# Kernel optimization log

Hardware: AMD Instinct MI355X
Metric: run time of the kernel (lower is better)

Reference implementation:

```python
import jax, jax.numpy as jnp
import numpy as np

B, S, E, H, Dh, R, L = 32, 512, 512, 8, 64, 3, 2
NI, NS = 10000, 1000
SCALE = float(1.0 / np.sqrt(Dh))
NEG = -1000000000.0


def _tensor_attn(q, kv, Wq, bq, Wk, bk, Wv, bv, Wg, bg, Wtq, btq, Wtk, btk, core, mask):
    # q, kv: [B,S,E]
    Q = q @ Wq + bq
    K = kv @ Wk + bk
    V = kv @ Wv + bv
    # per-query global bias computed from full key projection: [B,S,H] -> [B,H,S,1]
    glo = jnp.transpose(K @ Wg + bg, (0, 2, 1))[..., None]
    Qh = Q.reshape(B, S, H, Dh).transpose(0, 2, 1, 3)  # [B,H,S,Dh]
    Kh = K.reshape(B, S, H, Dh).transpose(0, 2, 1, 3)
    Vh = V.reshape(B, S, H, Dh).transpose(0, 2, 1, 3)
    scores = jnp.einsum('bhqd,bhkd->bhqk', Qh, Kh)  # [B,H,S,S]
    # low-rank bilinear tensor-core term; note it depends only on position s
    qt = Qh @ Wtq + btq  # [B,H,S,R]
    kt = Kh @ Wtk + btk  # [B,H,S,R]
    ts = jnp.einsum('bhsi,ij,bhsj->bhs', qt, core, kt)  # [B,H,S]
    scores = (scores + glo + ts[..., None]) * SCALE
    scores = jnp.where(mask, NEG, scores)
    p = jax.nn.softmax(scores, axis=-1)
    out = jnp.einsum('bhqk,bhkd->bhqd', p, Vh)
    return out.transpose(0, 2, 1, 3).reshape(B, S, E)


def setup_inputs() -> dict:
    key = jax.random.key(0)
    ks = jax.random.split(key, 24)
    f = lambda k, shp, s=0.02: (jax.random.normal(k, shp, dtype=jnp.float32) * s)
    inp = {}
    inp['item_inputs'] = jax.random.randint(ks[0], (B, S), 0, NI)
    inp['skill_inputs'] = jax.random.randint(ks[1], (B, S), 0, NS)
    inp['label_inputs'] = jax.random.randint(ks[2], (B, S), 0, 2)
    inp['item_ids'] = jax.random.randint(ks[3], (B, S), 0, NI)
    inp['skill_ids'] = jax.random.randint(ks[4], (B, S), 0, NS)
    inp['item_emb'] = f(ks[5], (NI + 1, E // 2), 1.0).at[0].set(0.0)  # padding_idx=0
    inp['skill_emb'] = f(ks[6], (NS + 1, E // 2), 1.0).at[0].set(0.0)
    inp['W_in'] = f(ks[7], (2 * E, E))
    inp['b_in'] = jnp.zeros((E,), jnp.float32)
    inp['Wq'] = f(ks[8], (L, E, E))
    inp['bq'] = jnp.zeros((L, E), jnp.float32)
    inp['Wk'] = f(ks[9], (L, E, E))
    inp['bk'] = jnp.zeros((L, E), jnp.float32)
    inp['Wv'] = f(ks[10], (L, E, E))
    inp['bv'] = jnp.zeros((L, E), jnp.float32)
    inp['Wg'] = f(ks[11], (L, E, H))
    inp['bg'] = jnp.zeros((L, H), jnp.float32)
    inp['Wtq'] = f(ks[12], (L, Dh, R), 0.1)
    inp['btq'] = jnp.zeros((L, R), jnp.float32)
    inp['Wtk'] = f(ks[13], (L, Dh, R), 0.1)
    inp['btk'] = jnp.zeros((L, R), jnp.float32)
    inp['core'] = f(ks[14], (L, R, R), 0.5)
    inp['W_out'] = f(ks[15], (E, 1))
    inp['b_out'] = jnp.zeros((1,), jnp.float32)
    return inp


def reference(item_inputs, skill_inputs, label_inputs, item_ids, skill_ids,
              item_emb, skill_emb, W_in, b_in, Wq, bq, Wk, bk, Wv, bv,
              Wg, bg, Wtq, btq, Wtk, btk, core, W_out, b_out):
    # get_inputs
    ie = item_emb[item_inputs]    # [B,S,E/2]
    se = skill_emb[skill_inputs]
    lab = label_inputs[..., None].astype(jnp.float32)
    half = jnp.concatenate([ie, se], axis=-1)  # [B,S,E]
    inputs = jnp.concatenate([half * lab, half * (1.0 - lab)], axis=-1)  # [B,S,2E]
    x = jax.nn.relu(inputs @ W_in + b_in)  # [B,S,E]
    # query
    query = jnp.concatenate([item_emb[item_ids], skill_emb[skill_ids]], axis=-1)
    mask = jnp.triu(jnp.ones((1, 1, S, S), dtype=bool), k=1)
    out = _tensor_attn(query, x, Wq[0], bq[0], Wk[0], bk[0], Wv[0], bv[0],
                       Wg[0], bg[0], Wtq[0], btq[0], Wtk[0], btk[0], core[0], mask)
    for l in range(1, L):
        res = _tensor_attn(query, out, Wq[l], bq[l], Wk[l], bk[l], Wv[l], bv[l],
                           Wg[l], bg[l], Wtq[l], btq[l], Wtk[l], btk[l], core[l], mask)
        out = out + jax.nn.relu(res)
    return out @ W_out + b_out  # [B,S,1]
```

## Files before the change

kernel.cpp:

```cpp
#include <hip/hip_runtime.h>
#include <stdint.h>


typedef short short8v __attribute__((ext_vector_type(8)));
typedef float f32x4 __attribute__((ext_vector_type(4)));

__device__ __forceinline__ float bf2f(unsigned short u) {
  union { unsigned int i; float f; } c;
  c.i = ((unsigned int)u) << 16;
  return c.f;
}
__device__ __forceinline__ unsigned short f2bf(float f) {
  union { float f; unsigned int i; } c;
  c.f = f;
  unsigned int u = c.i + 0x7FFFu + ((c.i >> 16) & 1u);
  return (unsigned short)(u >> 16);
}

__device__ __forceinline__ void g2l16(const void* g, void* l) {
  __builtin_amdgcn_global_load_lds(
      (const __attribute__((address_space(1))) unsigned int*)g,
      (__attribute__((address_space(3))) unsigned int*)l, 16, 0, 0);
}

struct WPtrs {
  const float* s[7];
  unsigned short* d[7];
};
__global__ __launch_bounds__(256) void transpose_all_k(WPtrs p, int* __restrict__ iperm) {
  int by = blockIdx.y;
  if (by == 0) {
    int gid = blockIdx.x * 256 + threadIdx.x;
    for (int i = gid; i < 16512; i += 4096) iperm[i] = 16384 + (i & 127);
  }
  __shared__ float t[32][33];
  int mi, r0t;
  if (by < 32) { mi = 0; r0t = by; }
  else { mi = 1 + ((by - 32) >> 4); r0t = (by - 32) & 15; }
  const float* in = p.s[mi];
  unsigned short* out = p.d[mi];
  int R = (mi == 0) ? 1024 : 512;
  const int C = 512;
  int c0 = blockIdx.x * 32, r0 = r0t * 32;
  int lr = threadIdx.x >> 5, lc = threadIdx.x & 31;
#pragma unroll
  for (int i = 0; i < 4; ++i) {
    int r = lr + i * 8;
    t[r][lc] = in[(size_t)(r0 + r) * C + (c0 + lc)];
  }
  __syncthreads();
#pragma unroll
  for (int i = 0; i < 4; ++i) {
    int r = lr + i * 8;
    out[(size_t)(c0 + r) * R + (r0 + lc)] = f2bf(t[lc][r]);
  }
}

__global__ __launch_bounds__(256) void scan_k(const int* __restrict__ label_in,
                                              int* __restrict__ iperm,
                                              int* __restrict__ rowpos,
                                              int* __restrict__ cnt) {
  __shared__ int sc[256];
  int t = threadIdx.x;
  int c = 0;
#pragma unroll 16
  for (int i = 0; i < 64; ++i) c += label_in[t * 64 + i];
  sc[t] = c;
  __syncthreads();
  for (int off = 1; off < 256; off <<= 1) {
    int v = sc[t];
    int u = (t >= off) ? sc[t - off] : 0;
    __syncthreads();
    sc[t] = v + u;
    __syncthreads();
  }
  int inc = sc[t];
  int ex = inc - c;
  int ex0 = t * 64 - ex;
  int p1 = ex;
  int p0 = 16511 - ex0;
  for (int i = 0; i < 64; ++i) {
    int row = t * 64 + i;
    int lb = label_in[row];
    int pos = lb ? (p1++) : (p0--);
    iperm[pos] = row;
    rowpos[row] = pos;
  }
  if (t == 255) cnt[0] = sc[255];
}

__global__ __launch_bounds__(256) void build_inputs_k(
    const int* __restrict__ item_in, const int* __restrict__ skill_in,
    const int* __restrict__ item_id, const int* __restrict__ skill_id,
    const float* __restrict__ iemb, const float* __restrict__ semb,
    unsigned short* __restrict__ HALFC, unsigned short* __restrict__ QRY,
    const int* __restrict__ rowpos) {
  int w = threadIdx.x >> 6, lane = threadIdx.x & 63;
  int row = blockIdx.x * 4 + w;
  int ii = item_in[row], si = skill_in[row];
  int iq = item_id[row], sq = skill_id[row];
  int pos = rowpos[row];
  int c = lane * 8;
  const float* src = (c < 256) ? (iemb + (size_t)ii * 256 + c)
                               : (semb + (size_t)si * 256 + (c - 256));
  union { unsigned short u[8]; int4 v; } o;
#pragma unroll
  for (int i = 0; i < 8; ++i) o.u[i] = f2bf(src[i]);
  *(int4*)(HALFC + (size_t)pos * 512 + c) = o.v;
  int qc = lane * 8;
  const float* qs = (qc < 256) ? (iemb + (size_t)iq * 256 + qc)
                               : (semb + (size_t)sq * 256 + (qc - 256));
  union { unsigned short u[8]; int4 v; } q;
#pragma unroll
  for (int i = 0; i < 8; ++i) q.u[i] = f2bf(qs[i]);
  *(int4*)(QRY + (size_t)row * 512 + qc) = q.v;
}

#define CT_LD 132

__global__ __launch_bounds__(256, 4) void gemm_q_in_k(
    const unsigned short* __restrict__ QRY, const unsigned short* __restrict__ WqTC,
    unsigned short* __restrict__ Qb, const unsigned short* __restrict__ HALFC,
    const unsigned short* __restrict__ WInT, unsigned short* __restrict__ X,
    const int* __restrict__ iperm, const int* __restrict__ cnt,
    const float* __restrict__ b_in, const float* __restrict__ bq, float SC) {
  __shared__ __align__(16) unsigned short uS[128 * CT_LD];
  int bid = blockIdx.x;
  int tid = threadIdx.x;
  int w = tid >> 6, lane = tid & 63, l16 = lane & 15, quad = lane >> 4;
  if (bid < 1024) {
    unsigned short* sA = uS;
    unsigned short* sB = uS + 128 * 64;
    unsigned short* Ct = uS;
    int mb = bid & 127, nb = bid >> 7;
    int wm = w & 1, wn = w >> 1;
    f32x4 acc[4][4];
#pragma unroll
    for (int i = 0; i < 4; ++i)
#pragma unroll
      for (int j = 0; j < 4; ++j) acc[i][j] = (f32x4){0.f, 0.f, 0.f, 0.f};
    for (int k0 = 0; k0 < 512; k0 += 64) {
      __syncthreads();
#pragma unroll
      for (int jj = 0; jj < 4; ++jj) {
        int c = jj * 256 + tid;
        int row = c >> 3, kc = c & 7, src = kc ^ (row & 7);
        g2l16(QRY + (size_t)(mb * 128 + row) * 512 + k0 + src * 8, sA + (size_t)c * 8);
      }
#pragma unroll
      for (int jj = 0; jj < 4; ++jj) {
        int c = jj * 256 + tid;
        int row = c >> 3, kc = c & 7, src = kc ^ (row & 7);
        g2l16(WqTC + (size_t)(nb * 128 + row) * 512 + k0 + src * 8, sB + (size_t)c * 8);
      }
      __syncthreads();
#pragma unroll
      for (int kk = 0; kk < 2; ++kk) {
        short8v aF[4], bF[4];
#pragma unroll
        for (int mt = 0; mt < 4; ++mt) {
          int r = wm * 64 + mt * 16 + l16;
          aF[mt] = *(const short8v*)(sA + r * 64 + (((kk * 4 + quad) ^ (r & 7)) << 3));
        }
#pragma unroll
        for (int nt = 0; nt < 4; ++nt) {
          int r = wn * 64 + nt * 16 + l16;
          bF[nt] = *(const short8v*)(sB + r * 64 + (((kk * 4 + quad) ^ (r & 7)) << 3));
        }
#pragma unroll
        for (int mt = 0; mt < 4; ++mt)
#pragma unroll
          for (int nt = 0; nt < 4; ++nt)
            acc[mt][nt] =
                __builtin_amdgcn_mfma_f32_16x16x32_bf16(aF[mt], bF[nt], acc[mt][nt], 0, 0, 0);
      }
    }
    __syncthreads();
#pragma unroll
    for (int mt = 0; mt < 4; ++mt)
#pragma unroll
      for (int nt = 0; nt < 4; ++nt) {
        int col = wn * 64 + nt * 16 + l16;
        float bs = bq[nb * 128 + col];
#pragma unroll
        for (int r = 0; r < 4; ++r) {
          int row = wm * 64 + mt * 16 + quad * 4 + r;
          Ct[row * CT_LD + col] = f2bf((acc[mt][nt][r] + bs) * SC);
        }
      }
    __syncthreads();
#pragma unroll
    for (int it = 0; it < 8; ++it) {
      int row = it * 16 + (tid >> 4);
      int col8 = (tid & 15) * 8;
      *(int4*)(Qb + (size_t)(mb * 128 + row) * 1024 + nb * 128 + col8) =
          *(const int4*)(Ct + row * CT_LD + col8);
    }
  } else {
    unsigned short* sA = uS;
    unsigned short* sB = uS + 64 * 64;
    unsigned short* Ct = uS;
    int id = bid - 1024;
    int nb = id / 264, mb = id % 264;
    if (mb >= 258) return;
    int n1 = *cnt;
    int koff = (mb < ((n1 + 63) >> 6)) ? 0 : 512;
    f32x4 acc[4][2];
#pragma unroll
    for (int i = 0; i < 4; ++i)
#pragma unroll
      for (int j = 0; j < 2; ++j) acc[i][j] = (f32x4){0.f, 0.f, 0.f, 0.f};
    for (int k0 = 0; k0 < 512; k0 += 64) {
      __syncthreads();
#pragma unroll
      for (int jj = 0; jj < 2; ++jj) {
        int c = jj * 256 + tid;
        int row = c >> 3, kc = c & 7, src = kc ^ (row & 7);
        g2l16(HALFC + (size_t)(mb * 64 + row) * 512 + k0 + src * 8, sA + (size_t)c * 8);
      }
#pragma unroll
      for (int jj = 0; jj < 4; ++jj) {
        int c = jj * 256 + tid;
        int row = c >> 3, kc = c & 7, src = kc ^ (row & 7);
        g2l16(WInT + (size_t)(nb * 128 + row) * 1024 + koff + k0 + src * 8, sB + (size_t)c * 8);
      }
      __syncthreads();
#pragma unroll
      for (int kk = 0; kk < 2; ++kk) {
        short8v aF[4], bF[2];
#pragma unroll
        for (int mt = 0; mt < 4; ++mt) {
          int r = mt * 16 + l16;
          aF[mt] = *(const short8v*)(sA + r * 64 + (((kk * 4 + quad) ^ (r & 7)) << 3));
        }
#pragma unroll
        for (int nt = 0; nt < 2; ++nt) {
          int r = w * 32 + nt * 16 + l16;
          bF[nt] = *(const short8v*)(sB + r * 64 + (((kk * 4 + quad) ^ (r & 7)) << 3));
        }
#pragma unroll
        for (int mt = 0; mt < 4; ++mt)
#pragma unroll
          for (int nt = 0; nt < 2; ++nt)
            acc[mt][nt] =
                __builtin_amdgcn_mfma_f32_16x16x32_bf16(aF[mt], bF[nt], acc[mt][nt], 0, 0, 0);
      }
    }
    __syncthreads();
#pragma unroll
    for (int mt = 0; mt < 4; ++mt)
#pragma unroll
      for (int nt = 0; nt < 2; ++nt) {
        int col = w * 32 + nt * 16 + l16;
        float bs = b_in[nb * 128 + col];
#pragma unroll
        for (int r = 0; r < 4; ++r) {
          int row = mt * 16 + quad * 4 + r;
          Ct[row * CT_LD + col] = f2bf(fmaxf(acc[mt][nt][r] + bs, 0.f));
        }
      }
    __syncthreads();
#pragma unroll
    for (int it = 0; it < 4; ++it) {
      int row = it * 16 + (tid >> 4);
      int tgt = iperm[mb * 64 + row];
      int col8 = (tid & 15) * 8;
      *(int4*)(X + (size_t)tgt * 512 + nb * 128 + col8) = *(const int4*)(Ct + row * CT_LD + col8);
    }
  }
}

__global__ __launch_bounds__(256, 4) void gemm_bt_k(
    const unsigned short* __restrict__ A, const unsigned short* __restrict__ Bt,
    unsigned short* __restrict__ C, int K, int ldc,
    const float* __restrict__ biasA, const float* __restrict__ biasB,
    int nsplit, float scale, unsigned short* __restrict__ VTout,
    float* __restrict__ dstfill, const float* __restrict__ bout) {
  __shared__ __align__(16) unsigned short uS[128 * CT_LD];
  unsigned short* sA = uS;
  unsigned short* sB = uS + 128 * 64;
  unsigned short* Ct = uS;
  int mb = blockIdx.x, nb = blockIdx.y;
  int tid = threadIdx.x;
  int w = tid >> 6, lane = tid & 63, l16 = lane & 15, quad = lane >> 4;
  int wm = w & 1, wn = w >> 1;
  if (dstfill && nb == 0 && tid < 128) dstfill[mb * 128 + tid] = bout[0];
  f32x4 acc[4][4];
#pragma unroll
  for (int i = 0; i < 4; ++i)
#pragma unroll
    for (int jn = 0; jn < 4; ++jn) acc[i][jn] = (f32x4){0.f, 0.f, 0.f, 0.f};

  for (int k0 = 0; k0 < K; k0 += 64) {
    __syncthreads();
#pragma unroll
    for (int jj = 0; jj < 4; ++jj) {
      int c = jj * 256 + tid;
      int row = c >> 3, kc = c & 7, src = kc ^ (row & 7);
      g2l16(A + (size_t)(mb * 128 + row) * K + k0 + src * 8, sA + (size_t)c * 8);
    }
#pragma unroll
    for (int jj = 0; jj < 4; ++jj) {
      int c = jj * 256 + tid;
      int row = c >> 3, kc = c & 7, src = kc ^ (row & 7);
      g2l16(Bt + (size_t)(nb * 128 + row) * K + k0 + src * 8, sB + (size_t)c * 8);
    }
    __syncthreads();
#pragma unroll
    for (int kk = 0; kk < 2; ++kk) {
      short8v aF[4], bF[4];
#pragma unroll
      for (int mt = 0; mt < 4; ++mt) {
        int r = wm * 64 + mt * 16 + l16;
        aF[mt] = *(const short8v*)(sA + r * 64 + (((kk * 4 + quad) ^ (r & 7)) << 3));
      }
#pragma unroll
      for (int nt = 0; nt < 4; ++nt) {
        int r = wn * 64 + nt * 16 + l16;
        bF[nt] = *(const short8v*)(sB + r * 64 + (((kk * 4 + quad) ^ (r & 7)) << 3));
      }
#pragma unroll
      for (int mt = 0; mt < 4; ++mt)
#pragma unroll
        for (int nt = 0; nt < 4; ++nt)
          acc[mt][nt] =
              __builtin_amdgcn_mfma_f32_16x16x32_bf16(aF[mt], bF[nt], acc[mt][nt], 0, 0, 0);
    }
  }
  __syncthreads();
#pragma unroll
  for (int mt = 0; mt < 4; ++mt)
#pragma unroll
    for (int nt = 0; nt < 4; ++nt) {
      int col = wn * 64 + nt * 16 + l16;
      int gcol = nb * 128 + col;
      float bs = (gcol < nsplit) ? biasA[gcol] : biasB[gcol - nsplit];
#pragma unroll
      for (int r = 0; r < 4; ++r) {
        int row = wm * 64 + mt * 16 + quad * 4 + r;
        Ct[row * CT_LD + col] = f2bf((acc[mt][nt][r] + bs) * scale);
      }
    }
  __syncthreads();
  if (VTout && nb >= 4) {
    int bb = mb >> 2, kpb = (mb & 3) * 128;
#pragma unroll
    for (int it = 0; it < 8; ++it) {
      int idx = it * 256 + tid;
      int dloc = idx >> 4, rem = idx & 15;
      union { unsigned short u[8]; int4 v; } o;
#pragma unroll
      for (int s = 0; s < 8; ++s) {
        int r = 32 * (rem >> 2) + 16 * (s >> 2) + 4 * (rem & 3) + (s & 3);
        o.u[s] = Ct[r * CT_LD + dloc];
      }
      *(int4*)(VTout + (size_t)(bb * 512 + (nb - 4) * 128 + dloc) * 512 + kpb + rem * 8) = o.v;
    }
  } else {
#pragma unroll
    for (int it = 0; it < 8; ++it) {
      int row = it * 16 + (tid >> 4);
      int col8 = (tid & 15) * 8;
      *(int4*)(C + (size_t)(mb * 128 + row) * ldc + nb * 128 + col8) =
          *(const int4*)(Ct + row * CT_LD + col8);
    }
  }
}

template <int FINAL>
__global__ __launch_bounds__(256, 4) void attn_k(const unsigned short* __restrict__ Qb,
                                                 int ldq,
                                                 const unsigned short* __restrict__ KVb,
                                                 const unsigned short* __restrict__ VT,
                                                 unsigned short* __restrict__ Out,
                                                 const unsigned short* __restrict__ out0,
                                                 const float* __restrict__ wout,
                                                 float* __restrict__ dst) {
  __shared__ __align__(16) unsigned short sK[64 * 64];
  __shared__ __align__(16) unsigned short sV[64 * 64];
  int tid = threadIdx.x;
  int w = tid >> 6, lane = tid & 63;
  int l16 = lane & 15, quad = lane >> 4;
  int bh = blockIdx.x;
  int b = bh >> 3, h = bh & 7;
  int jb = 7 - (int)blockIdx.y;
  int qb = jb * 64 + w * 16;
  f32x4 zf = {0.f, 0.f, 0.f, 0.f};
  short8v onesF;
#pragma unroll
  for (int i = 0; i < 8; ++i) onesF[i] = (short)0x3F80;

  short8v qF[2];
#pragma unroll
  for (int hf = 0; hf < 2; ++hf)
    qF[hf] = *(const short8v*)(Qb + (size_t)(b * 512 + qb + l16) * ldq + h * 64 + hf * 32 +
                               quad * 8);

  f32x4 O[4], RS = zf;
#pragma unroll
  for (int dt = 0; dt < 4; ++dt) O[dt] = zf;

  const unsigned short* Kg = KVb + (size_t)(b * 512) * 1024 + h * 64;
  const unsigned short* Vg = VT + (size_t)(bh * 64) * 512;

  for (int kt = 0; kt <= jb; ++kt) {
    __syncthreads();
#pragma unroll
    for (int jj = 0; jj < 2; ++jj) {
      int c = jj * 256 + tid;
      int row = c >> 3, kc = c & 7, src = kc ^ (row & 7);
      g2l16(Kg + (size_t)(kt * 64 + row) * 1024 + src * 8, sK + c * 8);
    }
#pragma unroll
    for (int jj = 0; jj < 2; ++jj) {
      int c = jj * 256 + tid;
      int row = c >> 3, kc = c & 7, src = kc ^ (row & 7);
      g2l16(Vg + (size_t)row * 512 + kt * 64 + src * 8, sV + c * 8);
    }
    __syncthreads();
#pragma unroll
    for (int kp = 0; kp < 2; ++kp) {
      int kb32 = kt * 64 + kp * 32;
      if (kb32 > qb) continue;
      short8v kC[2][2], vC[4];
#pragma unroll
      for (int v = 0; v < 2; ++v) {
        int r = kp * 32 + v * 16 + l16;
#pragma unroll
        for (int hf = 0; hf < 2; ++hf)
          kC[v][hf] = *(const short8v*)(sK + r * 64 + (((hf * 4 + quad) ^ (r & 7)) << 3));
      }
#pragma unroll
      for (int dt = 0; dt < 4; ++dt) {
        int r = dt * 16 + l16;
        vC[dt] = *(const short8v*)(sV + r * 64 + (((kp * 4 + quad) ^ (r & 7)) << 3));
      }
      f32x4 S[2];
#pragma unroll
      for (int v = 0; v < 2; ++v) {
        f32x4 s0 = __builtin_amdgcn_mfma_f32_16x16x32_bf16(kC[v][0], qF[0], zf, 0, 0, 0);
        S[v] = __builtin_amdgcn_mfma_f32_16x16x32_bf16(kC[v][1], qF[1], s0, 0, 0, 0);
      }
      if (kb32 + 31 > qb) {
#pragma unroll
        for (int v = 0; v < 2; ++v)
#pragma unroll
          for (int r = 0; r < 4; ++r)
            if (kb32 + v * 16 + quad * 4 + r > qb + l16) S[v][r] = -1e30f;
      }
      union { unsigned int u32[4]; short8v v8; } pk;
#pragma unroll
      for (int i = 0; i < 4; ++i) {
        int v = i >> 1, r0 = (i & 1) * 2;
        float e0 = __expf(S[v][r0]);
        float e1 = __expf(S[v][r0 + 1]);
        pk.u32[i] = (__float_as_uint(e0) >> 16) | (__float_as_uint(e1) & 0xFFFF0000u);
      }
#pragma unroll
      for (int dt = 0; dt < 4; ++dt)
        O[dt] = __builtin_amdgcn_mfma_f32_16x16x32_bf16(pk.v8, vC[dt], O[dt], 0, 0, 0);
      RS = __builtin_amdgcn_mfma_f32_16x16x32_bf16(pk.v8, onesF, RS, 0, 0, 0);
    }
  }
  float lr[4];
#pragma unroll
  for (int r = 0; r < 4; ++r) lr[r] = 1.f / RS[r];
  if (!FINAL) {
#pragma unroll
    for (int dt = 0; dt < 4; ++dt)
#pragma unroll
      for (int r = 0; r < 4; ++r)
        Out[(size_t)(b * 512 + qb + quad * 4 + r) * 512 + h * 64 + dt * 16 + l16] =
            f2bf(O[dt][r] * lr[r]);
  } else {
    float s[4] = {0.f, 0.f, 0.f, 0.f};
#pragma unroll
    for (int dt = 0; dt < 4; ++dt) {
      float wv = wout[h * 64 + dt * 16 + l16];
#pragma unroll
      for (int r = 0; r < 4; ++r) {
        float rv = bf2f(f2bf(O[dt][r] * lr[r]));
        float oo = bf2f(out0[(size_t)(b * 512 + qb + quad * 4 + r) * 512 + h * 64 +
                             dt * 16 + l16]);
        s[r] += (oo + fmaxf(rv, 0.f)) * wv;
      }
    }
#pragma unroll
    for (int off = 1; off < 16; off <<= 1)
#pragma unroll
      for (int r = 0; r < 4; ++r) s[r] += __shfl_xor(s[r], off);
    if (l16 == 0) {
#pragma unroll
      for (int r = 0; r < 4; ++r)
        atomicAdd(dst + b * 512 + qb + quad * 4 + r, s[r]);
    }
  }
}

extern "C" void kernel_launch(void* const* d_in, const int* in_sizes, int n_in,
                              void* d_out, int out_size, void* d_ws, size_t ws_size,
                              hipStream_t stream) {
  (void)in_sizes; (void)n_in; (void)out_size; (void)ws_size;
  const int* item_inputs = (const int*)d_in[0];
  const int* skill_inputs = (const int*)d_in[1];
  const int* label_inputs = (const int*)d_in[2];
  const int* item_ids = (const int*)d_in[3];
  const int* skill_ids = (const int*)d_in[4];
  const float* item_emb = (const float*)d_in[5];
  const float* skill_emb = (const float*)d_in[6];
  const float* W_in = (const float*)d_in[7];
  const float* b_in = (const float*)d_in[8];
  const float* Wq = (const float*)d_in[9];
  const float* bq = (const float*)d_in[10];
  const float* Wk = (const float*)d_in[11];
  const float* bk = (const float*)d_in[12];
  const float* Wv = (const float*)d_in[13];
  const float* bv = (const float*)d_in[14];
  const float* W_out = (const float*)d_in[22];
  const float* b_out = (const float*)d_in[23];

  unsigned short* ws = (unsigned short*)d_ws;
  unsigned short* HALFC = ws;
  unsigned short* OUT0 = ws;
  unsigned short* QRY = ws + (size_t)16512 * 512;
  unsigned short* X = QRY + (size_t)16384 * 512;
  unsigned short* Qb = X + (size_t)16512 * 512;
  unsigned short* KVb = Qb + (size_t)16384 * 1024;
  unsigned short* WInT = KVb + (size_t)16384 * 1024;
  unsigned short* WqTC = WInT + 512 * 1024;
  unsigned short* WkvT0 = WqTC + (size_t)1024 * 512;
  unsigned short* WkvT1 = WkvT0 + (size_t)1024 * 512;
  unsigned short* VT = WkvT1 + (size_t)1024 * 512;
  int* IPERM = (int*)(VT + (size_t)16384 * 512);
  int* CNT = IPERM + 16512;
  int* ROWPOS = CNT + 2;

  WPtrs p;
  p.s[0] = W_in;           p.d[0] = WInT;
  p.s[1] = Wq;             p.d[1] = WqTC;
  p.s[2] = Wq + 262144;    p.d[2] = WqTC + 512 * 512;
  p.s[3] = Wk;             p.d[3] = WkvT0;
  p.s[4] = Wv;             p.d[4] = WkvT0 + 262144;
  p.s[5] = Wk + 262144;    p.d[5] = WkvT1;
  p.s[6] = Wv + 262144;    p.d[6] = WkvT1 + 262144;
  transpose_all_k<<<dim3(16, 128), 256, 0, stream>>>(p, IPERM);

  scan_k<<<1, 256, 0, stream>>>(label_inputs, IPERM, ROWPOS, CNT);

  build_inputs_k<<<4096, 256, 0, stream>>>(item_inputs, skill_inputs, item_ids, skill_ids,
                                           item_emb, skill_emb, HALFC, QRY, ROWPOS);

  const float SC = 0.125f;
  gemm_q_in_k<<<2080, 256, 0, stream>>>(QRY, WqTC, Qb, HALFC, WInT, X, IPERM, CNT, b_in, bq,
                                        SC);
  gemm_bt_k<<<dim3(128, 8), 256, 0, stream>>>(X, WkvT0, KVb, 512, 1024, bk, bv, 512, 1.0f,
                                              VT, nullptr, nullptr);
  attn_k<0><<<dim3(256, 8), 256, 0, stream>>>(Qb, 1024, KVb, VT, OUT0, nullptr, nullptr,
                                              nullptr);
  gemm_bt_k<<<dim3(128, 8), 256, 0, stream>>>(OUT0, WkvT1, KVb, 512, 1024, bk + 512,
                                              bv + 512, 512, 1.0f, VT, (float*)d_out, b_out);
  attn_k<1><<<dim3(256, 8), 256, 0, stream>>>(Qb + 512, 1024, KVb, VT, nullptr, OUT0, W_out,
                                              (float*)d_out);
}
```

Baseline: 257.2 us.

## Double-buffer attention K/V tiles and merge transpose with input-build launch

The attention kernel now uses two LDS buffers for K and V. It issues the global-to-LDS loads for the next tile before computing the current one, using explicit vmcnt waits, barriers and setprio so load latency overlaps with MFMA work. The weight transpose and embedding gather kernels are merged into one launch. The iperm padding init moves into the scan kernel so it only fills the tail entries. This removes one kernel launch and a per-tile load stall, at the cost of doubling attention LDS use, which may reduce occupancy.

```diff
diff --git a/kernel.cpp b/kernel.cpp
--- a/kernel.cpp
+++ b/kernel.cpp
@@ -21,39 +21,6 @@
   __builtin_amdgcn_global_load_lds(
       (const __attribute__((address_space(1))) unsigned int*)g,
       (__attribute__((address_space(3))) unsigned int*)l, 16, 0, 0);
-}
-
-struct WPtrs {
-  const float* s[7];
-  unsigned short* d[7];
-};
-__global__ __launch_bounds__(256) void transpose_all_k(WPtrs p, int* __restrict__ iperm) {
-  int by = blockIdx.y;
-  if (by == 0) {
-    int gid = blockIdx.x * 256 + threadIdx.x;
-    for (int i = gid; i < 16512; i += 4096) iperm[i] = 16384 + (i & 127);
-  }
-  __shared__ float t[32][33];
-  int mi, r0t;
-  if (by < 32) { mi = 0; r0t = by; }
-  else { mi = 1 + ((by - 32) >> 4); r0t = (by - 32) & 15; }
-  const float* in = p.s[mi];
-  unsigned short* out = p.d[mi];
-  int R = (mi == 0) ? 1024 : 512;
-  const int C = 512;
-  int c0 = blockIdx.x * 32, r0 = r0t * 32;
-  int lr = threadIdx.x >> 5, lc = threadIdx.x & 31;
-#pragma unroll
-  for (int i = 0; i < 4; ++i) {
-    int r = lr + i * 8;
-    t[r][lc] = in[(size_t)(r0 + r) * C + (c0 + lc)];
-  }
-  __syncthreads();
-#pragma unroll
-  for (int i = 0; i < 4; ++i) {
-    int r = lr + i * 8;
-    out[(size_t)(c0 + r) * R + (r0 + lc)] = f2bf(t[lc][r]);
-  }
 }
 
 __global__ __launch_bounds__(256) void scan_k(const int* __restrict__ label_in,
@@ -75,6 +42,7 @@
     __syncthreads();
   }
   int inc = sc[t];
+  int n1 = sc[255];
   int ex = inc - c;
   int ex0 = t * 64 - ex;
   int p1 = ex;
@@ -86,34 +54,65 @@
     iperm[pos] = row;
     rowpos[row] = pos;
   }
-  if (t == 255) cnt[0] = sc[255];
-}
-
-__global__ __launch_bounds__(256) void build_inputs_k(
-    const int* __restrict__ item_in, const int* __restrict__ skill_in,
+  if (t < 128) iperm[n1 + t] = 16384 + t;
+  if (t == 255) cnt[0] = n1;
+}
+
+struct WPtrs {
+  const float* s[7];
+  unsigned short* d[7];
+};
+__global__ __launch_bounds__(256) void trans_build_k(
+    WPtrs p, const int* __restrict__ item_in, const int* __restrict__ skill_in,
     const int* __restrict__ item_id, const int* __restrict__ skill_id,
     const float* __restrict__ iemb, const float* __restrict__ semb,
     unsigned short* __restrict__ HALFC, unsigned short* __restrict__ QRY,
     const int* __restrict__ rowpos) {
-  int w = threadIdx.x >> 6, lane = threadIdx.x & 63;
-  int row = blockIdx.x * 4 + w;
-  int ii = item_in[row], si = skill_in[row];
-  int iq = item_id[row], sq = skill_id[row];
-  int pos = rowpos[row];
-  int c = lane * 8;
-  const float* src = (c < 256) ? (iemb + (size_t)ii * 256 + c)
-                               : (semb + (size_t)si * 256 + (c - 256));
-  union { unsigned short u[8]; int4 v; } o;
-#pragma unroll
-  for (int i = 0; i < 8; ++i) o.u[i] = f2bf(src[i]);
-  *(int4*)(HALFC + (size_t)pos * 512 + c) = o.v;
-  int qc = lane * 8;
-  const float* qs = (qc < 256) ? (iemb + (size_t)iq * 256 + qc)
-                               : (semb + (size_t)sq * 256 + (qc - 256));
-  union { unsigned short u[8]; int4 v; } q;
-#pragma unroll
-  for (int i = 0; i < 8; ++i) q.u[i] = f2bf(qs[i]);
-  *(int4*)(QRY + (size_t)row * 512 + qc) = q.v;
+  int tb = blockIdx.x;
+  if (tb < 2048) {
+    __shared__ float t[32][33];
+    int by = tb >> 4, bx = tb & 15;
+    int mi, r0t;
+    if (by < 32) { mi = 0; r0t = by; }
+    else { mi = 1 + ((by - 32) >> 4); r0t = (by - 32) & 15; }
+    const float* in = p.s[mi];
+    unsigned short* out = p.d[mi];
+    int R = (mi == 0) ? 1024 : 512;
+    const int C = 512;
+    int c0 = bx * 32, r0 = r0t * 32;
+    int lr = threadIdx.x >> 5, lc = threadIdx.x & 31;
+#pragma unroll
+    for (int i = 0; i < 4; ++i) {
+      int r = lr + i * 8;
+      t[r][lc] = in[(size_t)(r0 + r) * C + (c0 + lc)];
+    }
+    __syncthreads();
+#pragma unroll
+    for (int i = 0; i < 4; ++i) {
+      int r = lr + i * 8;
+      out[(size_t)(c0 + r) * R + (r0 + lc)] = f2bf(t[lc][r]);
+    }
+  } else {
+    int bb = tb - 2048;
+    int w = threadIdx.x >> 6, lane = threadIdx.x & 63;
+    int row = bb * 4 + w;
+    int ii = item_in[row], si = skill_in[row];
+    int iq = item_id[row], sq = skill_id[row];
+    int pos = rowpos[row];
+    int c = lane * 8;
+    const float* src = (c < 256) ? (iemb + (size_t)ii * 256 + c)
+                                 : (semb + (size_t)si * 256 + (c - 256));
+    union { unsigned short u[8]; int4 v; } o;
+#pragma unroll
+    for (int i = 0; i < 8; ++i) o.u[i] = f2bf(src[i]);
+    *(int4*)(HALFC + (size_t)pos * 512 + c) = o.v;
+    const float* qs = (c < 256) ? (iemb + (size_t)iq * 256 + c)
+                                : (semb + (size_t)sq * 256 + (c - 256));
+    union { unsigned short u[8]; int4 v; } q;
+#pragma unroll
+    for (int i = 0; i < 8; ++i) q.u[i] = f2bf(qs[i]);
+    *(int4*)(QRY + (size_t)row * 512 + c) = q.v;
+  }
 }
 
 #define CT_LD 132
@@ -367,6 +366,20 @@
   }
 }
 
+#define ATTN_STAGE(kt, bf)                                                      \
+  {                                                                             \
+    _Pragma("unroll") for (int jj = 0; jj < 2; ++jj) {                          \
+      int c = jj * 256 + tid;                                                   \
+      int row = c >> 3, kc = c & 7, src = kc ^ (row & 7);                       \
+      g2l16(Kg + (size_t)((kt) * 64 + row) * 1024 + src * 8, &sK[bf][c * 8]);   \
+    }                                                                           \
+    _Pragma("unroll") for (int jj = 0; jj < 2; ++jj) {                          \
+      int c = jj * 256 + tid;                                                   \
+      int row = c >> 3, kc = c & 7, src = kc ^ (row & 7);                       \
+      g2l16(Vg + (size_t)row * 512 + (kt) * 64 + src * 8, &sV[bf][c * 8]);      \
+    }                                                                           \
+  }
+
 template <int FINAL>
 __global__ __launch_bounds__(256, 4) void attn_k(const unsigned short* __restrict__ Qb,
                                                  int ldq,
@@ -376,8 +389,8 @@
                                                  const unsigned short* __restrict__ out0,
                                                  const float* __restrict__ wout,
                                                  float* __restrict__ dst) {
-  __shared__ __align__(16) unsigned short sK[64 * 64];
-  __shared__ __align__(16) unsigned short sV[64 * 64];
+  __shared__ __align__(16) unsigned short sK[2][64 * 64];
+  __shared__ __align__(16) unsigned short sV[2][64 * 64];
   int tid = threadIdx.x;
   int w = tid >> 6, lane = tid & 63;
   int l16 = lane & 15, quad = lane >> 4;
@@ -390,6 +403,9 @@
 #pragma unroll
   for (int i = 0; i < 8; ++i) onesF[i] = (short)0x3F80;
 
+  const unsigned short* Kg = KVb + (size_t)(b * 512) * 1024 + h * 64;
+  const unsigned short* Vg = VT + (size_t)(bh * 64) * 512;
+
   short8v qF[2];
 #pragma unroll
   for (int hf = 0; hf < 2; ++hf)
@@ -400,24 +416,19 @@
 #pragma unroll
   for (int dt = 0; dt < 4; ++dt) O[dt] = zf;
 
-  const unsigned short* Kg = KVb + (size_t)(b * 512) * 1024 + h * 64;
-  const unsigned short* Vg = VT + (size_t)(bh * 64) * 512;
+  ATTN_STAGE(0, 0);
 
   for (int kt = 0; kt <= jb; ++kt) {
-    __syncthreads();
-#pragma unroll
-    for (int jj = 0; jj < 2; ++jj) {
-      int c = jj * 256 + tid;
-      int row = c >> 3, kc = c & 7, src = kc ^ (row & 7);
-      g2l16(Kg + (size_t)(kt * 64 + row) * 1024 + src * 8, sK + c * 8);
-    }
-#pragma unroll
-    for (int jj = 0; jj < 2; ++jj) {
-      int c = jj * 256 + tid;
-      int row = c >> 3, kc = c & 7, src = kc ^ (row & 7);
-      g2l16(Vg + (size_t)row * 512 + kt * 64 + src * 8, sV + c * 8);
-    }
-    __syncthreads();
+    int cur = kt & 1;
+    if (kt < jb) {
+      ATTN_STAGE(kt + 1, cur ^ 1);
+      asm volatile("s_waitcnt vmcnt(4)" ::: "memory");
+    } else {
+      asm volatile("s_waitcnt vmcnt(0)" ::: "memory");
+    }
+    __builtin_amdgcn_sched_barrier(0);
+    __builtin_amdgcn_s_barrier();
+    __builtin_amdgcn_s_setprio(1);
 #pragma unroll
     for (int kp = 0; kp < 2; ++kp) {
       int kb32 = kt * 64 + kp * 32;
@@ -428,12 +439,12 @@
         int r = kp * 32 + v * 16 + l16;
 #pragma unroll
         for (int hf = 0; hf < 2; ++hf)
-          kC[v][hf] = *(const short8v*)(sK + r * 64 + (((hf * 4 + quad) ^ (r & 7)) << 3));
+          kC[v][hf] = *(const short8v*)(&sK[cur][r * 64 + (((hf * 4 + quad) ^ (r & 7)) << 3)]);
       }
 #pragma unroll
       for (int dt = 0; dt < 4; ++dt) {
         int r = dt * 16 + l16;
-        vC[dt] = *(const short8v*)(sV + r * 64 + (((kp * 4 + quad) ^ (r & 7)) << 3));
+        vC[dt] = *(const short8v*)(&sV[cur][r * 64 + (((kp * 4 + quad) ^ (r & 7)) << 3)]);
       }
       f32x4 S[2];
 #pragma unroll
@@ -461,6 +472,8 @@
         O[dt] = __builtin_amdgcn_mfma_f32_16x16x32_bf16(pk.v8, vC[dt], O[dt], 0, 0, 0);
       RS = __builtin_amdgcn_mfma_f32_16x16x32_bf16(pk.v8, onesF, RS, 0, 0, 0);
     }
+    __builtin_amdgcn_s_setprio(0);
+    __builtin_amdgcn_s_barrier();
   }
   float lr[4];
 #pragma unroll
@@ -543,12 +556,10 @@
   p.s[4] = Wv;             p.d[4] = WkvT0 + 262144;
   p.s[5] = Wk + 262144;    p.d[5] = WkvT1;
   p.s[6] = Wv + 262144;    p.d[6] = WkvT1 + 262144;
-  transpose_all_k<<<dim3(16, 128), 256, 0, stream>>>(p, IPERM);
 
   scan_k<<<1, 256, 0, stream>>>(label_inputs, IPERM, ROWPOS, CNT);
-
-  build_inputs_k<<<4096, 256, 0, stream>>>(item_inputs, skill_inputs, item_ids, skill_ids,
-                                           item_emb, skill_emb, HALFC, QRY, ROWPOS);
+  trans_build_k<<<6144, 256, 0, stream>>>(p, item_inputs, skill_inputs, item_ids, skill_ids,
+                                          item_emb, skill_emb, HALFC, QRY, ROWPOS);
 
   const float SC = 0.125f;
   gemm_q_in_k<<<2080, 256, 0, stream>>>(QRY, WqTC, Qb, HALFC, WInT, X, IPERM, CNT, b_in, bq,
```

Result: slower. 268.4 us (+4.4%).
